# Performance work log

Hardware: AMD Instinct MI355X
Metric: run time of the kernel (lower is better)

## Reference

```python
import jax, jax.numpy as jnp
import numpy as np
import math

N, E = 1000, 128000
IN_DIM, HID, OUT_DIM = 256, 512, 16
L, H = 6, 8
C = HID // H  # 64, TransformerConv out_channels per head
EDGE_DIM = 32
MAX_LEN = 1000


def _pe(max_len, d_model):
    pos = np.arange(max_len)[:, None].astype(np.float32)
    div = np.exp(np.arange(0, d_model, 2).astype(np.float32) * (-math.log(10000.0) / d_model))
    pe = np.zeros((max_len, d_model), dtype=np.float32)
    pe[:, 0::2] = np.sin(pos * div)
    pe[:, 1::2] = np.cos(pos * div)
    return jnp.asarray(pe)


def setup_inputs() -> dict:
    key = jax.random.key(0)
    ks = jax.random.split(key, 32)
    g = lambda k, shape, fan_in: jax.random.normal(k, shape, jnp.float32) / jnp.sqrt(jnp.float32(fan_in))
    inp = {
        "x": jax.random.normal(ks[0], (N, IN_DIM), jnp.float32),
        "edge_index": jax.random.randint(ks[1], (2, E), 0, N, jnp.int64 if jax.config.jax_enable_x64 else jnp.int32),
        "edge_attr": jax.random.uniform(ks[2], (E, 4), jnp.float32),
        "embed_w": g(ks[3], (IN_DIM, HID), IN_DIM),
        "embed_b": jnp.zeros((HID,), jnp.float32),
        "pe": _pe(MAX_LEN, HID),
        "ee_w1": g(ks[4], (4, 16), 4), "ee_b1": jnp.zeros((16,), jnp.float32),
        "ee_w2": g(ks[5], (16, EDGE_DIM), 16), "ee_b2": jnp.zeros((EDGE_DIM,), jnp.float32),
        "q_w": g(ks[6], (L, HID, HID), HID), "q_b": jnp.zeros((L, HID), jnp.float32),
        "k_w": g(ks[7], (L, HID, HID), HID), "k_b": jnp.zeros((L, HID), jnp.float32),
        "v_w": g(ks[8], (L, HID, HID), HID), "v_b": jnp.zeros((L, HID), jnp.float32),
        "e_w": g(ks[9], (L, EDGE_DIM, HID), EDGE_DIM),
        "skip_w": g(ks[10], (L, HID, HID), HID), "skip_b": jnp.zeros((L, HID), jnp.float32),
        "ln_g": jnp.ones((L, HID), jnp.float32), "ln_b": jnp.zeros((L, HID), jnp.float32),
        "dom_w": g(ks[11], (HID, 16), HID), "dom_b": jnp.zeros((16,), jnp.float32),
        "cls_w1": g(ks[12], (HID + 16, HID // 2), HID + 16), "cls_b1": jnp.zeros((HID // 2,), jnp.float32),
        "cls_w2": g(ks[13], (HID // 2, OUT_DIM), HID // 2), "cls_b2": jnp.zeros((OUT_DIM,), jnp.float32),
    }
    return inp


def _layer_norm(x, g, b, eps=1e-5):
    mu = jnp.mean(x, axis=-1, keepdims=True)
    var = jnp.var(x, axis=-1, keepdims=True)
    return (x - mu) * jax.lax.rsqrt(var + eps) * g + b


def _forward(x, edge_index, edge_attr, embed_w, embed_b, pe, ee_w1, ee_b1, ee_w2, ee_b2,
             q_w, q_b, k_w, k_b, v_w, v_b, e_w, skip_w, skip_b, ln_g, ln_b,
             dom_w, dom_b, cls_w1, cls_b1, cls_w2, cls_b2):
    n = x.shape[0]
    h = x @ embed_w + embed_b
    h = h + pe[:n]
    # edge encoder: 4 -> 16 -> 32
    ef = jax.nn.relu(edge_attr @ ee_w1 + ee_b1) @ ee_w2 + ee_b2  # [E, 32]
    src, tgt = edge_index[0], edge_index[1]
    scale = 1.0 / math.sqrt(C)
    for l in range(L):
        res = h
        q = (h @ q_w[l] + q_b[l]).reshape(n, H, C)
        k = (h @ k_w[l] + k_b[l]).reshape(n, H, C)
        v = (h @ v_w[l] + v_b[l]).reshape(n, H, C)
        e = (ef @ e_w[l]).reshape(-1, H, C)            # [E, H, C], lin_edge has no bias
        kj = k[src] + e                                 # gather + edge bias
        score = jnp.sum(q[tgt] * kj, axis=-1) * scale   # [E, H]
        # segment softmax over incoming edges of each target node
        m = jax.ops.segment_max(score, tgt, num_segments=n)     # [N, H]
        al = jnp.exp(score - m[tgt])
        den = jax.ops.segment_sum(al, tgt, num_segments=n)      # [N, H]
        al = al / den[tgt]
        msg = (v[src] + e) * al[:, :, None]             # [E, H, C]
        out = jax.ops.segment_sum(msg, tgt, num_segments=n).reshape(n, HID)
        out = out + h @ skip_w[l] + skip_b[l]           # root_weight skip
        h = _layer_norm(out + res, ln_g[l], ln_b[l])
    dom = h @ dom_w + dom_b                             # [N, 16]
    comb = jnp.concatenate([h, dom], axis=-1)
    hid = jax.nn.relu(comb @ cls_w1 + cls_b1)
    return hid @ cls_w2 + cls_b2


def reference(x, edge_index, edge_attr, embed_w, embed_b, pe, ee_w1, ee_b1, ee_w2, ee_b2,
              q_w, q_b, k_w, k_b, v_w, v_b, e_w, skip_w, skip_b, ln_g, ln_b,
              dom_w, dom_b, cls_w1, cls_b1, cls_w2, cls_b2):
    return _forward(x, edge_index, edge_attr, embed_w, embed_b, pe, ee_w1, ee_b1, ee_w2, ee_b2,
                    q_w, q_b, k_w, k_b, v_w, v_b, e_w, skip_w, skip_b, ln_g, ln_b,
                    dom_w, dom_b, cls_w1, cls_b1, cls_w2, cls_b2)
```

## Files before the change

### kernel.cpp

```cpp
#include <hip/hip_runtime.h>
#include <hip/hip_bf16.h>
#include <cstdint>
#include <cstddef>

#define NN 1000
#define EE 128000
#define LAYERS 6
#define SCALE 0.125f
#define MAXDEG 320

typedef __attribute__((ext_vector_type(4))) float f32x4;
typedef __attribute__((ext_vector_type(8))) short short8v;

static __device__ __forceinline__ unsigned short f2bf(float x){
    unsigned int u = __float_as_uint(x);
    unsigned int lsb = (u >> 16) & 1u;
    u += 0x7fffu + lsb;
    return (unsigned short)(u >> 16);
}

__global__ void zero_counts(int* cnt){
    cnt[threadIdx.x] = 0;
}

__global__ void hist_kernel(const int* __restrict__ tgt, int* cnt){
    int e = blockIdx.x*256 + threadIdx.x;
    if (e < EE) atomicAdd(&cnt[tgt[e]], 1);
}

__global__ void scan_kernel(const int* __restrict__ cnt, int* offs, int* cursor){
    __shared__ int s[1024];
    int tid = threadIdx.x;
    s[tid] = (tid < NN) ? cnt[tid] : 0;
    __syncthreads();
    for (int st = 1; st < 1024; st <<= 1){
        int v = (tid >= st) ? s[tid-st] : 0;
        __syncthreads();
        s[tid] += v;
        __syncthreads();
    }
    int excl = (tid == 0) ? 0 : s[tid-1];
    if (tid < NN){ offs[tid] = excl; cursor[tid] = excl; }
    if (tid == 0) offs[NN] = s[NN-1];
}

__global__ void scatter_kernel(const int* __restrict__ src, const int* __restrict__ tgt,
                               int* cursor, int* ssrc, int* epos){
    int e = blockIdx.x*256 + threadIdx.x;
    if (e < EE){
        int t = tgt[e];
        int pos = atomicAdd(&cursor[t], 1);
        ssrc[pos] = src[e];
        epos[e] = pos;
    }
}

__global__ __launch_bounds__(256) void edge_enc(
    const float* __restrict__ edge_attr,
    const float* __restrict__ w1, const float* __restrict__ b1,
    const float* __restrict__ w2, const float* __restrict__ b2,
    const int* __restrict__ epos,
    float* __restrict__ efs)
{
    __shared__ float w1s[64], b1s[16], w2s[512], b2s[32];
    int tid = threadIdx.x;
    if (tid < 64) w1s[tid] = w1[tid];
    if (tid < 16) b1s[tid] = b1[tid];
    if (tid < 32) b2s[tid] = b2[tid];
    w2s[tid] = w2[tid];
    w2s[tid+256] = w2[tid+256];
    __syncthreads();
    int e = blockIdx.x*256 + tid;
    if (e >= EE) return;
    float4 av = *(const float4*)(edge_attr + (size_t)e*4);
    float hd[16];
    #pragma unroll
    for (int i = 0; i < 16; i++){
        float v = av.x*w1s[i] + av.y*w1s[16+i] + av.z*w1s[32+i] + av.w*w1s[48+i] + b1s[i];
        hd[i] = fmaxf(v, 0.f);
    }
    float outv[32];
    #pragma unroll
    for (int k = 0; k < 32; k++){
        float v = b2s[k];
        #pragma unroll
        for (int i = 0; i < 16; i++) v += hd[i]*w2s[i*32+k];
        outv[k] = v;
    }
    float* op = efs + (size_t)epos[e]*32;
    #pragma unroll
    for (int k4 = 0; k4 < 8; k4++){
        *(float4*)(op + k4*4) = make_float4(outv[k4*4], outv[k4*4+1], outv[k4*4+2], outv[k4*4+3]);
    }
}

__global__ __launch_bounds__(256) void convert_x(const float* __restrict__ x, unsigned short* __restrict__ xb){
    int row = blockIdx.x;
    int c = threadIdx.x;
    xb[(size_t)row*256 + c] = (row < NN) ? f2bf(x[(size_t)row*256 + c]) : (unsigned short)0;
}

__global__ __launch_bounds__(256) void tconv(const float* __restrict__ src, unsigned short* __restrict__ dst,
                                             int Kk, int Nn){
    int tn = blockIdx.x, tk = blockIdx.y;
    __shared__ float ts[32][33];
    int tid = threadIdx.x;
    int r = tid >> 3, c0 = (tid & 7)*4;
    float4 v = *(const float4*)(src + (size_t)(tk*32 + r)*Nn + tn*32 + c0);
    ts[r][c0+0] = v.x; ts[r][c0+1] = v.y; ts[r][c0+2] = v.z; ts[r][c0+3] = v.w;
    __syncthreads();
    ushort4 o;
    o.x = f2bf(ts[c0+0][r]); o.y = f2bf(ts[c0+1][r]);
    o.z = f2bf(ts[c0+2][r]); o.w = f2bf(ts[c0+3][r]);
    *(ushort4*)(dst + (size_t)(tn*32 + r)*Kk + tk*32 + c0) = o;
}

__global__ __launch_bounds__(256) void tconv24(
    const float* __restrict__ Wq, const float* __restrict__ Wk,
    const float* __restrict__ Wv, const float* __restrict__ Ws,
    unsigned short* __restrict__ Wt)
{
    int bid = blockIdx.x;
    int mm = bid >> 8;
    int tile = bid & 255;
    int tk = tile >> 4, tn = tile & 15;
    int l = mm >> 2, m = mm & 3;
    const float* W = ((m==0)?Wq:(m==1)?Wk:(m==2)?Wv:Ws) + (size_t)l*512*512;
    unsigned short* dst = Wt + (size_t)mm*512*512;
    __shared__ float ts[32][33];
    int tid = threadIdx.x;
    int r = tid >> 3, c0 = (tid & 7)*4;
    float4 v = *(const float4*)(W + (size_t)(tk*32 + r)*512 + tn*32 + c0);
    ts[r][c0+0] = v.x; ts[r][c0+1] = v.y; ts[r][c0+2] = v.z; ts[r][c0+3] = v.w;
    __syncthreads();
    ushort4 o;
    o.x = f2bf(ts[c0+0][r]); o.y = f2bf(ts[c0+1][r]);
    o.z = f2bf(ts[c0+2][r]); o.w = f2bf(ts[c0+3][r]);
    *(ushort4*)(dst + (size_t)(tn*32 + r)*512 + tk*32 + c0) = o;
}

__global__ __launch_bounds__(256) void gemm_embed_mfma(
    const unsigned short* __restrict__ xb,
    const unsigned short* __restrict__ ewt,
    const float* __restrict__ bias, const float* __restrict__ pe,
    float* __restrict__ C, unsigned short* __restrict__ hb)
{
    int bid = blockIdx.x;
    int mt = bid >> 2, nt = bid & 3;
    int row0 = mt*64, col0 = nt*128;

    __shared__ __align__(16) unsigned short As[64*40];
    __shared__ __align__(16) unsigned short Bs[128*40];

    int tid = threadIdx.x;
    int wid = tid >> 6, l = tid & 63;
    int wm = wid >> 1, wn = wid & 1;

    f32x4 acc[2][4] = {};
    int ar = tid >> 2, akq = tid & 3;
    for (int k0 = 0; k0 < 256; k0 += 32){
        *(uint4*)&As[ar*40 + akq*8]      = *(const uint4*)&xb[(size_t)(row0+ar)*256 + k0 + akq*8];
        *(uint4*)&Bs[ar*40 + akq*8]      = *(const uint4*)&ewt[(size_t)(col0+ar)*256 + k0 + akq*8];
        *(uint4*)&Bs[(ar+64)*40 + akq*8] = *(const uint4*)&ewt[(size_t)(col0+ar+64)*256 + k0 + akq*8];
        __syncthreads();
        short8v a0 = *(const short8v*)&As[(wm*32 + (l&15))*40 + (l>>4)*8];
        short8v a1 = *(const short8v*)&As[(wm*32 + 16 + (l&15))*40 + (l>>4)*8];
        #pragma unroll
        for (int nj = 0; nj < 4; nj++){
            short8v b = *(const short8v*)&Bs[(wn*64 + nj*16 + (l&15))*40 + (l>>4)*8];
            acc[0][nj] = __builtin_amdgcn_mfma_f32_16x16x32_bf16(a0, b, acc[0][nj], 0, 0, 0);
            acc[1][nj] = __builtin_amdgcn_mfma_f32_16x16x32_bf16(a1, b, acc[1][nj], 0, 0, 0);
        }
        __syncthreads();
    }
    int rbase = (l >> 4)*4, cl = l & 15;
    #pragma unroll
    for (int mi = 0; mi < 2; mi++)
        #pragma unroll
        for (int nj = 0; nj < 4; nj++)
            #pragma unroll
            for (int r = 0; r < 4; r++){
                int grow = row0 + wm*32 + mi*16 + rbase + r;
                int gcol = col0 + wn*64 + nj*16 + cl;
                if (grow < NN){
                    float v = acc[mi][nj][r] + bias[gcol] + pe[(size_t)grow*512 + gcol];
                    C[(size_t)grow*512 + gcol] = v;
                    hb[(size_t)grow*512 + gcol] = f2bf(v);
                }
            }
}

__global__ __launch_bounds__(256) void gemm_qkvs_mfma(
    const unsigned short* __restrict__ hb,
    const unsigned short* __restrict__ Wt,
    const float* __restrict__ qb, const float* __restrict__ kb,
    const float* __restrict__ vb, const float* __restrict__ sb,
    float* __restrict__ Q, float* __restrict__ K,
    float* __restrict__ V, float* __restrict__ S)
{
    int bid = blockIdx.x;
    int mat = bid >> 6;
    int rem = bid & 63;
    int mt = rem >> 2, nt = rem & 3;
    int row0 = mt*64, col0 = nt*128;
    const unsigned short* W = Wt + (size_t)mat*512*512;
    const float* bias = (mat==0)?qb:(mat==1)?kb:(mat==2)?vb:sb;
    float* C = (mat==0)?Q:(mat==1)?K:(mat==2)?V:S;

    __shared__ __align__(16) unsigned short As[64*72];
    __shared__ __align__(16) unsigned short Bs[128*72];

    int tid = threadIdx.x;
    int wid = tid >> 6, l = tid & 63;
    int wm = wid >> 1, wn = wid & 1;

    f32x4 acc[2][4] = {};
    int ar = tid >> 2, ac = tid & 3;
    int br = tid >> 1, bc = tid & 1;
    for (int k0 = 0; k0 < 512; k0 += 64){
        *(uint4*)&As[ar*72 + ac*16 + 0] = *(const uint4*)&hb[(size_t)(row0+ar)*512 + k0 + ac*16 + 0];
        *(uint4*)&As[ar*72 + ac*16 + 8] = *(const uint4*)&hb[(size_t)(row0+ar)*512 + k0 + ac*16 + 8];
        #pragma unroll
        for (int j = 0; j < 4; j++)
            *(uint4*)&Bs[br*72 + bc*32 + j*8] = *(const uint4*)&W[(size_t)(col0+br)*512 + k0 + bc*32 + j*8];
        __syncthreads();
        #pragma unroll
        for (int ks = 0; ks < 64; ks += 32){
            short8v a0 = *(const short8v*)&As[(wm*32 + (l&15))*72 + ks + (l>>4)*8];
            short8v a1 = *(const short8v*)&As[(wm*32 + 16 + (l&15))*72 + ks + (l>>4)*8];
            #pragma unroll
            for (int nj = 0; nj < 4; nj++){
                short8v b = *(const short8v*)&Bs[(wn*64 + nj*16 + (l&15))*72 + ks + (l>>4)*8];
                acc[0][nj] = __builtin_amdgcn_mfma_f32_16x16x32_bf16(a0, b, acc[0][nj], 0, 0, 0);
                acc[1][nj] = __builtin_amdgcn_mfma_f32_16x16x32_bf16(a1, b, acc[1][nj], 0, 0, 0);
            }
        }
        __syncthreads();
    }
    int rbase = (l >> 4)*4, cl = l & 15;
    #pragma unroll
    for (int mi = 0; mi < 2; mi++)
        #pragma unroll
        for (int nj = 0; nj < 4; nj++)
            #pragma unroll
            for (int r = 0; r < 4; r++){
                int grow = row0 + wm*32 + mi*16 + rbase + r;
                int gcol = col0 + wn*64 + nj*16 + cl;
                if (grow < NN) C[(size_t)grow*512 + gcol] = acc[mi][nj][r] + bias[gcol];
            }
}

__global__ __launch_bounds__(512) void attn_layer(
    const float* __restrict__ hcur,
    const float* __restrict__ Qm, const float* __restrict__ Km,
    const float* __restrict__ Vm, const float* __restrict__ SKm,
    const float* __restrict__ efs, const float* __restrict__ e_w_l,
    const float* __restrict__ ln_g_l, const float* __restrict__ ln_b_l,
    const int* __restrict__ ssrc, const int* __restrict__ offs,
    float* __restrict__ hnext, unsigned short* __restrict__ hbn)
{
    int tid = threadIdx.x;
    int t = blockIdx.x;

    __shared__ float q_s[8*68];
    __shared__ float qe_s[8*36];
    __shared__ float sc_s[MAXDEG*8];
    __shared__ __align__(8) unsigned short efb_s[MAXDEG*32];
    __shared__ int   src_s[MAXDEG];
    __shared__ float pv_s[2048];
    __shared__ float pe_s[512];
    __shared__ float s_s[256];
    __shared__ float red[64], red2[64];
    __shared__ float m_s[8], d_s[8];

    q_s[(tid>>6)*68 + (tid&63)] = Qm[(size_t)t*512 + tid];
    __syncthreads();
    if (tid < 256){
        int hh = tid>>5, dd = tid&31;
        const float* wrow = e_w_l + (size_t)dd*512 + hh*64;
        const float* qh = q_s + hh*68;
        float a = 0.f;
        #pragma unroll
        for (int c = 0; c < 64; c++) a += qh[c]*wrow[c];
        qe_s[hh*36 + dd] = a;
    }
    int start = offs[t], deg = offs[t+1] - start;
    __syncthreads();

    int cw = tid >> 5, l = tid & 31;
    int h = l >> 2, sub = l & 3;
    const float4* qp4  = (const float4*)(q_s + h*68 + sub*16);
    const float4* qep4 = (const float4*)(qe_s + h*36 + sub*8);
    float4 qa0 = qp4[0], qa1 = qp4[1], qa2 = qp4[2], qa3 = qp4[3];
    float4 qe0 = qep4[0], qe1 = qep4[1];
    float lmax = -1e30f;
    for (int i = cw; i < deg; i += 16){
        int s = ssrc[start + i];
        if (l == 0) src_s[i] = s;
        const float4* kr = (const float4*)(Km + (size_t)s*512 + l*16);
        const float4* er = (const float4*)(efs + (size_t)(start+i)*32);
        float4 k0 = kr[0], k1 = kr[1], k2 = kr[2], k3 = kr[3];
        float4 e0 = er[sub*2], e1 = er[sub*2+1];
        float p;
        p  = qa0.x*k0.x + qa0.y*k0.y + qa0.z*k0.z + qa0.w*k0.w;
        p += qa1.x*k1.x + qa1.y*k1.y + qa1.z*k1.z + qa1.w*k1.w;
        p += qa2.x*k2.x + qa2.y*k2.y + qa2.z*k2.z + qa2.w*k2.w;
        p += qa3.x*k3.x + qa3.y*k3.y + qa3.z*k3.z + qa3.w*k3.w;
        p += qe0.x*e0.x + qe0.y*e0.y + qe0.z*e0.z + qe0.w*e0.w;
        p += qe1.x*e1.x + qe1.y*e1.y + qe1.z*e1.z + qe1.w*e1.w;
        p += __shfl_xor(p, 1);
        p += __shfl_xor(p, 2);
        p *= SCALE;
        lmax = fmaxf(lmax, p);
        if (sub == 0) sc_s[i*8 + h] = p;
        if (l < 8){
            float4 ev = er[l];
            ushort4 ub;
            ub.x = f2bf(ev.x); ub.y = f2bf(ev.y); ub.z = f2bf(ev.z); ub.w = f2bf(ev.w);
            *(ushort4*)&efb_s[i*32 + l*4] = ub;
        }
    }
    lmax = fmaxf(lmax, __shfl_xor(lmax, 32));
    if (((tid & 63) < 32) && sub == 0) red[(tid>>6)*8 + h] = lmax;
    __syncthreads();
    if (tid < 8){
        float m = red[tid];
        #pragma unroll
        for (int w = 1; w < 8; w++) m = fmaxf(m, red[w*8 + tid]);
        m_s[tid] = m;
    }
    __syncthreads();

    {
        int he = tid & 7, ie = tid >> 3;
        float mh = m_s[he];
        float den = 0.f;
        for (int i = ie; i < deg; i += 64){
            float al = __expf(sc_s[i*8 + he] - mh);
            sc_s[i*8 + he] = al;
            den += al;
        }
        den += __shfl_xor(den, 8);
        den += __shfl_xor(den, 16);
        den += __shfl_xor(den, 32);
        if ((tid & 63) < 8) red2[(tid>>6)*8 + (tid & 7)] = den;
    }
    __syncthreads();
    if (tid < 8){
        float d = 0.f;
        #pragma unroll
        for (int w = 0; w < 8; w++) d += red2[w*8 + tid];
        d_s[tid] = d;
    }
    __syncthreads();

    {
        int c4 = tid & 127, g = tid >> 7;
        int h2 = c4 >> 4;
        float4 acc = make_float4(0.f, 0.f, 0.f, 0.f);
        const float4* Vm4 = (const float4*)Vm;
        #pragma unroll 4
        for (int i = g; i < deg; i += 4){
            int s = src_s[i];
            float al = sc_s[i*8 + h2];
            float4 v = Vm4[(size_t)s*128 + c4];
            acc.x += al*v.x; acc.y += al*v.y; acc.z += al*v.z; acc.w += al*v.w;
        }
        *(float4*)&pv_s[g*512 + c4*4] = acc;
    }
    {
        int c2 = tid & 255, g2 = tid >> 8;
        int h3 = c2 >> 5, dd3 = c2 & 31;
        float accE = 0.f;
        #pragma unroll 8
        for (int i = g2; i < deg; i += 2){
            float al = sc_s[i*8 + h3];
            float ev = __uint_as_float(((unsigned)efb_s[i*32 + dd3]) << 16);
            accE += al * ev;
        }
        pe_s[g2*256 + c2] = accE;
    }
    __syncthreads();
    if (tid < 256){
        float dv = d_s[tid>>5];
        float invd = (dv > 0.f) ? 1.f/dv : 0.f;
        s_s[tid] = (pe_s[tid] + pe_s[256+tid]) * invd;
    }
    __syncthreads();

    int c = tid;
    int hh2 = c >> 6;
    float dv = d_s[hh2];
    float invd = (dv > 0.f) ? 1.f/dv : 0.f;
    float vtot = pv_s[c] + pv_s[512+c] + pv_s[1024+c] + pv_s[1536+c];
    float r = vtot * invd;
    float oe = 0.f;
    const float* sp = s_s + hh2*32;
    #pragma unroll
    for (int d = 0; d < 32; d++) oe += sp[d]*e_w_l[(size_t)d*512 + c];
    float x = r + oe + SKm[(size_t)t*512 + c] + hcur[(size_t)t*512 + c];

    int wv = tid >> 6, ln = tid & 63;
    float sA = x, sB = x*x;
    #pragma unroll
    for (int m2 = 1; m2 <= 32; m2 <<= 1){
        sA += __shfl_xor(sA, m2);
        sB += __shfl_xor(sB, m2);
    }
    if (ln == 0){ red[wv] = sA; red2[wv] = sB; }
    __syncthreads();
    float tot = 0.f, tot2 = 0.f;
    #pragma unroll
    for (int w = 0; w < 8; w++){ tot += red[w]; tot2 += red2[w]; }
    float mu  = tot*(1.f/512.f);
    float var = tot2*(1.f/512.f) - mu*mu;
    float rstd = rsqrtf(var + 1e-5f);
    float y = (x - mu)*rstd*ln_g_l[c] + ln_b_l[c];
    hnext[(size_t)t*512 + c] = y;
    hbn[(size_t)t*512 + c]   = f2bf(y);
}

__global__ __launch_bounds__(256) void final_head(
    const float* __restrict__ hin,
    const float* __restrict__ dom_w, const float* __restrict__ dom_b,
    const float* __restrict__ w1, const float* __restrict__ b1,
    const float* __restrict__ w2, const float* __restrict__ b2,
    float* __restrict__ out)
{
    int tid = threadIdx.x, t = blockIdx.x;
    __shared__ float h_s[512];
    __shared__ float dom_s[16];
    __shared__ float hid_s[256];
    __shared__ float red[256];
    h_s[tid]     = hin[(size_t)t*512 + tid];
    h_s[tid+256] = hin[(size_t)t*512 + 256 + tid];
    __syncthreads();
    if (tid < 16){
        float a = dom_b[tid];
        for (int i = 0; i < 512; i++) a += h_s[i]*dom_w[i*16 + tid];
        dom_s[tid] = a;
    }
    __syncthreads();
    float acc = b1[tid];
    for (int i = 0; i < 512; i++) acc += h_s[i]*w1[(size_t)i*256 + tid];
    #pragma unroll
    for (int i = 0; i < 16; i++) acc += dom_s[i]*w1[(size_t)(512+i)*256 + tid];
    hid_s[tid] = fmaxf(acc, 0.f);
    __syncthreads();
    int o = tid & 15, g = tid >> 4;
    float p = 0.f;
    #pragma unroll
    for (int j = 0; j < 16; j++) p += hid_s[g*16 + j]*w2[(g*16 + j)*16 + o];
    red[tid] = p;
    __syncthreads();
    if (tid < 16){
        float s2 = b2[tid];
        for (int gg = 0; gg < 16; gg++) s2 += red[gg*16 + tid];
        out[(size_t)t*16 + tid] = s2;
    }
}

extern "C" void kernel_launch(void* const* d_in, const int* in_sizes, int n_in,
                              void* d_out, int out_size, void* d_ws, size_t ws_size,
                              hipStream_t stream)
{
    const float* x       = (const float*)d_in[0];
    const int*   eidx    = (const int*)  d_in[1];
    const float* eattr   = (const float*)d_in[2];
    const float* embed_w = (const float*)d_in[3];
    const float* embed_b = (const float*)d_in[4];
    const float* pe      = (const float*)d_in[5];
    const float* ee_w1   = (const float*)d_in[6];
    const float* ee_b1   = (const float*)d_in[7];
    const float* ee_w2   = (const float*)d_in[8];
    const float* ee_b2   = (const float*)d_in[9];
    const float* q_w     = (const float*)d_in[10];
    const float* q_b     = (const float*)d_in[11];
    const float* k_w     = (const float*)d_in[12];
    const float* k_b     = (const float*)d_in[13];
    const float* v_w     = (const float*)d_in[14];
    const float* v_b     = (const float*)d_in[15];
    const float* e_w     = (const float*)d_in[16];
    const float* skip_w  = (const float*)d_in[17];
    const float* skip_b  = (const float*)d_in[18];
    const float* ln_g    = (const float*)d_in[19];
    const float* ln_b    = (const float*)d_in[20];
    const float* dom_w   = (const float*)d_in[21];
    const float* dom_b   = (const float*)d_in[22];
    const float* cls_w1  = (const float*)d_in[23];
    const float* cls_b1  = (const float*)d_in[24];
    const float* cls_w2  = (const float*)d_in[25];
    const float* cls_b2  = (const float*)d_in[26];
    float* out = (float*)d_out;

    float* ws = (float*)d_ws;
    size_t o = 0;
    float* h0    = ws + o; o += (size_t)512*NN;
    float* h1    = ws + o; o += (size_t)512*NN;
    float* Qb    = ws + o; o += (size_t)512*NN;
    float* Kb    = ws + o; o += (size_t)512*NN;
    float* Vb    = ws + o; o += (size_t)512*NN;
    float* Sb    = ws + o; o += (size_t)512*NN;
    float* efs   = ws + o; o += (size_t)32*EE;
    unsigned short* hb  = (unsigned short*)(ws + o); o += (size_t)1024*512/2;
    unsigned short* xb  = (unsigned short*)(ws + o); o += (size_t)1024*256/2;
    unsigned short* ewt = (unsigned short*)(ws + o); o += (size_t)512*256/2;
    unsigned short* Wtb = (unsigned short*)(ws + o); o += (size_t)24*512*512/2;
    int* cnt    = (int*)(ws + o); o += 1024;
    int* offs   = (int*)(ws + o); o += 1024;
    int* cursor = (int*)(ws + o); o += 1024;
    int* ssrc   = (int*)(ws + o); o += EE;
    int* epos   = (int*)(ws + o); o += EE;

    const int* srcp = eidx;
    const int* tgtp = eidx + EE;

    zero_counts<<<1, 1024, 0, stream>>>(cnt);
    hist_kernel<<<EE/256, 256, 0, stream>>>(tgtp, cnt);
    scan_kernel<<<1, 1024, 0, stream>>>(cnt, offs, cursor);
    scatter_kernel<<<EE/256, 256, 0, stream>>>(srcp, tgtp, cursor, ssrc, epos);
    edge_enc<<<EE/256, 256, 0, stream>>>(eattr, ee_w1, ee_b1, ee_w2, ee_b2, epos, efs);
    convert_x<<<1024, 256, 0, stream>>>(x, xb);
    tconv<<<dim3(512/32, 256/32), 256, 0, stream>>>(embed_w, ewt, 256, 512);
    tconv24<<<24*256, 256, 0, stream>>>(q_w, k_w, v_w, skip_w, Wtb);
    gemm_embed_mfma<<<64, 256, 0, stream>>>(xb, ewt, embed_b, pe, h0, hb);

    float* hc = h0;
    float* hn = h1;
    for (int l = 0; l < LAYERS; l++){
        gemm_qkvs_mfma<<<256, 256, 0, stream>>>(
            hb, Wtb + (size_t)l*4*512*512,
            q_b + (size_t)l*512, k_b + (size_t)l*512,
            v_b + (size_t)l*512, skip_b + (size_t)l*512,
            Qb, Kb, Vb, Sb);
        attn_layer<<<NN, 512, 0, stream>>>(
            hc, Qb, Kb, Vb, Sb, efs, e_w + (size_t)l*32*512,
            ln_g + (size_t)l*512, ln_b + (size_t)l*512,
            ssrc, offs, hn, hb);
        float* tmp = hc; hc = hn; hn = tmp;
    }
    final_head<<<NN, 256, 0, stream>>>(hc, dom_w, dom_b, cls_w1, cls_b1, cls_w2, cls_b2, out);
}
```

Measured before the change: 684.2 us.

## Store K, V and edge features in bf16; retile QKVS GEMM with register prefetch

K and V projections and the encoded edge features are now written as bf16 instead of fp32, halving the gather traffic in the attention kernel. The attention kernel also drops its shared-memory bf16 copy of edge features and reads them from global memory. The QKVS GEMM switches to 64x64 tiles with twice as many blocks and prefetches the next K-slice into registers. The cost is lower precision in K and V, which were previously fp32.

```diff
diff --git a/kernel.cpp b/kernel.cpp
--- a/kernel.cpp
+++ b/kernel.cpp
@@ -17,6 +17,9 @@
     unsigned int lsb = (u >> 16) & 1u;
     u += 0x7fffu + lsb;
     return (unsigned short)(u >> 16);
+}
+static __device__ __forceinline__ float bf2f(unsigned short u){
+    return __uint_as_float(((unsigned int)u) << 16);
 }
 
 __global__ void zero_counts(int* cnt){
@@ -60,7 +63,7 @@
     const float* __restrict__ w1, const float* __restrict__ b1,
     const float* __restrict__ w2, const float* __restrict__ b2,
     const int* __restrict__ epos,
-    float* __restrict__ efs)
+    unsigned short* __restrict__ efs)
 {
     __shared__ float w1s[64], b1s[16], w2s[512], b2s[32];
     int tid = threadIdx.x;
@@ -79,18 +82,21 @@
         float v = av.x*w1s[i] + av.y*w1s[16+i] + av.z*w1s[32+i] + av.w*w1s[48+i] + b1s[i];
         hd[i] = fmaxf(v, 0.f);
     }
-    float outv[32];
-    #pragma unroll
-    for (int k = 0; k < 32; k++){
-        float v = b2s[k];
-        #pragma unroll
-        for (int i = 0; i < 16; i++) v += hd[i]*w2s[i*32+k];
-        outv[k] = v;
-    }
-    float* op = efs + (size_t)epos[e]*32;
+    unsigned short* op = efs + (size_t)epos[e]*32;
     #pragma unroll
     for (int k4 = 0; k4 < 8; k4++){
-        *(float4*)(op + k4*4) = make_float4(outv[k4*4], outv[k4*4+1], outv[k4*4+2], outv[k4*4+3]);
+        ushort4 ub;
+        float v0 = b2s[k4*4+0], v1 = b2s[k4*4+1], v2 = b2s[k4*4+2], v3 = b2s[k4*4+3];
+        #pragma unroll
+        for (int i = 0; i < 16; i++){
+            float hv = hd[i];
+            v0 += hv*w2s[i*32 + k4*4+0];
+            v1 += hv*w2s[i*32 + k4*4+1];
+            v2 += hv*w2s[i*32 + k4*4+2];
+            v3 += hv*w2s[i*32 + k4*4+3];
+        }
+        ub.x = f2bf(v0); ub.y = f2bf(v1); ub.z = f2bf(v2); ub.w = f2bf(v3);
+        *(ushort4*)(op + k4*4) = ub;
     }
 }
 
@@ -195,66 +201,84 @@
     const unsigned short* __restrict__ Wt,
     const float* __restrict__ qb, const float* __restrict__ kb,
     const float* __restrict__ vb, const float* __restrict__ sb,
-    float* __restrict__ Q, float* __restrict__ K,
-    float* __restrict__ V, float* __restrict__ S)
+    float* __restrict__ Q, unsigned short* __restrict__ K16,
+    unsigned short* __restrict__ V16, float* __restrict__ S)
 {
     int bid = blockIdx.x;
-    int mat = bid >> 6;
-    int rem = bid & 63;
-    int mt = rem >> 2, nt = rem & 3;
-    int row0 = mt*64, col0 = nt*128;
+    int mat = bid >> 7;
+    int rem = bid & 127;
+    int mt = rem >> 3, nt = rem & 7;
+    int row0 = mt*64, col0 = nt*64;
     const unsigned short* W = Wt + (size_t)mat*512*512;
     const float* bias = (mat==0)?qb:(mat==1)?kb:(mat==2)?vb:sb;
-    float* C = (mat==0)?Q:(mat==1)?K:(mat==2)?V:S;
 
     __shared__ __align__(16) unsigned short As[64*72];
-    __shared__ __align__(16) unsigned short Bs[128*72];
+    __shared__ __align__(16) unsigned short Bs[64*72];
 
     int tid = threadIdx.x;
     int wid = tid >> 6, l = tid & 63;
     int wm = wid >> 1, wn = wid & 1;
 
-    f32x4 acc[2][4] = {};
-    int ar = tid >> 2, ac = tid & 3;
-    int br = tid >> 1, bc = tid & 1;
+    f32x4 acc[2][2] = {};
+    int lr = tid >> 2;
+    int lc = (tid & 3)*2;
+    const unsigned short* ga = hb + (size_t)(row0+lr)*512 + lc*8;
+    const unsigned short* gb = W  + (size_t)(col0+lr)*512 + lc*8;
+
+    uint4 ra0 = *(const uint4*)(ga);
+    uint4 ra1 = *(const uint4*)(ga + 8);
+    uint4 rb0 = *(const uint4*)(gb);
+    uint4 rb1 = *(const uint4*)(gb + 8);
+
     for (int k0 = 0; k0 < 512; k0 += 64){
-        *(uint4*)&As[ar*72 + ac*16 + 0] = *(const uint4*)&hb[(size_t)(row0+ar)*512 + k0 + ac*16 + 0];
-        *(uint4*)&As[ar*72 + ac*16 + 8] = *(const uint4*)&hb[(size_t)(row0+ar)*512 + k0 + ac*16 + 8];
-        #pragma unroll
-        for (int j = 0; j < 4; j++)
-            *(uint4*)&Bs[br*72 + bc*32 + j*8] = *(const uint4*)&W[(size_t)(col0+br)*512 + k0 + bc*32 + j*8];
         __syncthreads();
-        #pragma unroll
-        for (int ks = 0; ks < 64; ks += 32){
-            short8v a0 = *(const short8v*)&As[(wm*32 + (l&15))*72 + ks + (l>>4)*8];
-            short8v a1 = *(const short8v*)&As[(wm*32 + 16 + (l&15))*72 + ks + (l>>4)*8];
-            #pragma unroll
-            for (int nj = 0; nj < 4; nj++){
-                short8v b = *(const short8v*)&Bs[(wn*64 + nj*16 + (l&15))*72 + ks + (l>>4)*8];
-                acc[0][nj] = __builtin_amdgcn_mfma_f32_16x16x32_bf16(a0, b, acc[0][nj], 0, 0, 0);
-                acc[1][nj] = __builtin_amdgcn_mfma_f32_16x16x32_bf16(a1, b, acc[1][nj], 0, 0, 0);
-            }
-        }
+        *(uint4*)&As[lr*72 + lc*8]     = ra0;
+        *(uint4*)&As[lr*72 + lc*8 + 8] = ra1;
+        *(uint4*)&Bs[lr*72 + lc*8]     = rb0;
+        *(uint4*)&Bs[lr*72 + lc*8 + 8] = rb1;
         __syncthreads();
+        if (k0 + 64 < 512){
+            ra0 = *(const uint4*)(ga + k0 + 64);
+            ra1 = *(const uint4*)(ga + k0 + 72);
+            rb0 = *(const uint4*)(gb + k0 + 64);
+            rb1 = *(const uint4*)(gb + k0 + 72);
+        }
+        #pragma unroll
+        for (int ks = 0; ks < 2; ks++){
+            short8v a0 = *(const short8v*)&As[(wm*32 + (l&15))*72      + ks*32 + (l>>4)*8];
+            short8v a1 = *(const short8v*)&As[(wm*32 + 16 + (l&15))*72 + ks*32 + (l>>4)*8];
+            short8v b0 = *(const short8v*)&Bs[(wn*32 + (l&15))*72      + ks*32 + (l>>4)*8];
+            short8v b1 = *(const short8v*)&Bs[(wn*32 + 16 + (l&15))*72 + ks*32 + (l>>4)*8];
+            acc[0][0] = __builtin_amdgcn_mfma_f32_16x16x32_bf16(a0, b0, acc[0][0], 0, 0, 0);
+            acc[0][1] = __builtin_amdgcn_mfma_f32_16x16x32_bf16(a0, b1, acc[0][1], 0, 0, 0);
+            acc[1][0] = __builtin_amdgcn_mfma_f32_16x16x32_bf16(a1, b0, acc[1][0], 0, 0, 0);
+            acc[1][1] = __builtin_amdgcn_mfma_f32_16x16x32_bf16(a1, b1, acc[1][1], 0, 0, 0);
+        }
     }
     int rbase = (l >> 4)*4, cl = l & 15;
     #pragma unroll
     for (int mi = 0; mi < 2; mi++)
         #pragma unroll
-        for (int nj = 0; nj < 4; nj++)
+        for (int nj = 0; nj < 2; nj++)
             #pragma unroll
             for (int r = 0; r < 4; r++){
                 int grow = row0 + wm*32 + mi*16 + rbase + r;
-                int gcol = col0 + wn*64 + nj*16 + cl;
-                if (grow < NN) C[(size_t)grow*512 + gcol] = acc[mi][nj][r] + bias[gcol];
+                int gcol = col0 + wn*32 + nj*16 + cl;
+                if (grow < NN){
+                    float v = acc[mi][nj][r] + bias[gcol];
+                    if (mat == 0)      Q[(size_t)grow*512 + gcol] = v;
+                    else if (mat == 1) K16[(size_t)grow*512 + gcol] = f2bf(v);
+                    else if (mat == 2) V16[(size_t)grow*512 + gcol] = f2bf(v);
+                    else               S[(size_t)grow*512 + gcol] = v;
+                }
             }
 }
 
 __global__ __launch_bounds__(512) void attn_layer(
     const float* __restrict__ hcur,
-    const float* __restrict__ Qm, const float* __restrict__ Km,
-    const float* __restrict__ Vm, const float* __restrict__ SKm,
-    const float* __restrict__ efs, const float* __restrict__ e_w_l,
+    const float* __restrict__ Qm, const unsigned short* __restrict__ Km,
+    const unsigned short* __restrict__ Vm, const float* __restrict__ SKm,
+    const unsigned short* __restrict__ efs, const float* __restrict__ e_w_l,
     const float* __restrict__ ln_g_l, const float* __restrict__ ln_b_l,
     const int* __restrict__ ssrc, const int* __restrict__ offs,
     float* __restrict__ hnext, unsigned short* __restrict__ hbn)
@@ -265,7 +289,6 @@
     __shared__ float q_s[8*68];
     __shared__ float qe_s[8*36];
     __shared__ float sc_s[MAXDEG*8];
-    __shared__ __align__(8) unsigned short efb_s[MAXDEG*32];
     __shared__ int   src_s[MAXDEG];
     __shared__ float pv_s[2048];
     __shared__ float pe_s[512];
@@ -297,28 +320,28 @@
     for (int i = cw; i < deg; i += 16){
         int s = ssrc[start + i];
         if (l == 0) src_s[i] = s;
-        const float4* kr = (const float4*)(Km + (size_t)s*512 + l*16);
-        const float4* er = (const float4*)(efs + (size_t)(start+i)*32);
-        float4 k0 = kr[0], k1 = kr[1], k2 = kr[2], k3 = kr[3];
-        float4 e0 = er[sub*2], e1 = er[sub*2+1];
+        const unsigned short* kr = Km + (size_t)s*512 + l*16;
+        short8v k0 = *(const short8v*)(kr);
+        short8v k1 = *(const short8v*)(kr + 8);
+        short8v ev = *(const short8v*)(efs + (size_t)(start+i)*32 + sub*8);
         float p;
-        p  = qa0.x*k0.x + qa0.y*k0.y + qa0.z*k0.z + qa0.w*k0.w;
-        p += qa1.x*k1.x + qa1.y*k1.y + qa1.z*k1.z + qa1.w*k1.w;
-        p += qa2.x*k2.x + qa2.y*k2.y + qa2.z*k2.z + qa2.w*k2.w;
-        p += qa3.x*k3.x + qa3.y*k3.y + qa3.z*k3.z + qa3.w*k3.w;
-        p += qe0.x*e0.x + qe0.y*e0.y + qe0.z*e0.z + qe0.w*e0.w;
-        p += qe1.x*e1.x + qe1.y*e1.y + qe1.z*e1.z + qe1.w*e1.w;
+        p  = qa0.x*bf2f((unsigned short)k0[0]) + qa0.y*bf2f((unsigned short)k0[1])
+           + qa0.z*bf2f((unsigned short)k0[2]) + qa0.w*bf2f((unsigned short)k0[3]);
+        p += qa1.x*bf2f((unsigned short)k0[4]) + qa1.y*bf2f((unsigned short)k0[5])
+           + qa1.z*bf2f((unsigned short)k0[6]) + qa1.w*bf2f((unsigned short)k0[7]);
+        p += qa2.x*bf2f((unsigned short)k1[0]) + qa2.y*bf2f((unsigned short)k1[1])
+           + qa2.z*bf2f((unsigned short)k1[2]) + qa2.w*bf2f((unsigned short)k1[3]);
+        p += qa3.x*bf2f((unsigned short)k1[4]) + qa3.y*bf2f((unsigned short)k1[5])
+           + qa3.z*bf2f((unsigned short)k1[6]) + qa3.w*bf2f((unsigned short)k1[7]);
+        p += qe0.x*bf2f((unsigned short)ev[0]) + qe0.y*bf2f((unsigned short)ev[1])
+           + qe0.z*bf2f((unsigned short)ev[2]) + qe0.w*bf2f((unsigned short)ev[3]);
+        p += qe1.x*bf2f((unsigned short)ev[4]) + qe1.y*bf2f((unsigned short)ev[5])
+           + qe1.z*bf2f((unsigned short)ev[6]) + qe1.w*bf2f((unsigned short)ev[7]);
         p += __shfl_xor(p, 1);
         p += __shfl_xor(p, 2);
         p *= SCALE;
         lmax = fmaxf(lmax, p);
         if (sub == 0) sc_s[i*8 + h] = p;
-        if (l < 8){
-            float4 ev = er[l];
-            ushort4 ub;
-            ub.x = f2bf(ev.x); ub.y = f2bf(ev.y); ub.z = f2bf(ev.z); ub.w = f2bf(ev.w);
-            *(ushort4*)&efb_s[i*32 + l*4] = ub;
-        }
     }
     lmax = fmaxf(lmax, __shfl_xor(lmax, 32));
     if (((tid & 63) < 32) && sub == 0) red[(tid>>6)*8 + h] = lmax;
@@ -358,13 +381,13 @@
         int c4 = tid & 127, g = tid >> 7;
         int h2 = c4 >> 4;
         float4 acc = make_float4(0.f, 0.f, 0.f, 0.f);
-        const float4* Vm4 = (const float4*)Vm;
         #pragma unroll 4
         for (int i = g; i < deg; i += 4){
             int s = src_s[i];
             float al = sc_s[i*8 + h2];
-            float4 v = Vm4[(size_t)s*128 + c4];
-            acc.x += al*v.x; acc.y += al*v.y; acc.z += al*v.z; acc.w += al*v.w;
+            ushort4 v = *(const ushort4*)(Vm + (size_t)s*512 + c4*4);
+            acc.x += al*bf2f(v.x); acc.y += al*bf2f(v.y);
+            acc.z += al*bf2f(v.z); acc.w += al*bf2f(v.w);
         }
         *(float4*)&pv_s[g*512 + c4*4] = acc;
     }
@@ -375,8 +398,7 @@
         #pragma unroll 8
         for (int i = g2; i < deg; i += 2){
             float al = sc_s[i*8 + h3];
-            float ev = __uint_as_float(((unsigned)efb_s[i*32 + dd3]) << 16);
-            accE += al * ev;
+            accE += al * bf2f(efs[(size_t)(start+i)*32 + dd3]);
         }
         pe_s[g2*256 + c2] = accE;
     }
@@ -498,14 +520,14 @@
     float* h0    = ws + o; o += (size_t)512*NN;
     float* h1    = ws + o; o += (size_t)512*NN;
     float* Qb    = ws + o; o += (size_t)512*NN;
-    float* Kb    = ws + o; o += (size_t)512*NN;
-    float* Vb    = ws + o; o += (size_t)512*NN;
     float* Sb    = ws + o; o += (size_t)512*NN;
-    float* efs   = ws + o; o += (size_t)32*EE;
-    unsigned short* hb  = (unsigned short*)(ws + o); o += (size_t)1024*512/2;
-    unsigned short* xb  = (unsigned short*)(ws + o); o += (size_t)1024*256/2;
-    unsigned short* ewt = (unsigned short*)(ws + o); o += (size_t)512*256/2;
-    unsigned short* Wtb = (unsigned short*)(ws + o); o += (size_t)24*512*512/2;
+    unsigned short* Kb16 = (unsigned short*)(ws + o); o += (size_t)1024*512/2;
+    unsigned short* Vb16 = (unsigned short*)(ws + o); o += (size_t)1024*512/2;
+    unsigned short* efs  = (unsigned short*)(ws + o); o += (size_t)EE*32/2;
+    unsigned short* hb   = (unsigned short*)(ws + o); o += (size_t)1024*512/2;
+    unsigned short* xb   = (unsigned short*)(ws + o); o += (size_t)1024*256/2;
+    unsigned short* ewt  = (unsigned short*)(ws + o); o += (size_t)512*256/2;
+    unsigned short* Wtb  = (unsigned short*)(ws + o); o += (size_t)24*512*512/2;
     int* cnt    = (int*)(ws + o); o += 1024;
     int* offs   = (int*)(ws + o); o += 1024;
     int* cursor = (int*)(ws + o); o += 1024;
@@ -528,13 +550,13 @@
     float* hc = h0;
     float* hn = h1;
     for (int l = 0; l < LAYERS; l++){
-        gemm_qkvs_mfma<<<256, 256, 0, stream>>>(
+        gemm_qkvs_mfma<<<512, 256, 0, stream>>>(
             hb, Wtb + (size_t)l*4*512*512,
             q_b + (size_t)l*512, k_b + (size_t)l*512,
             v_b + (size_t)l*512, skip_b + (size_t)l*512,
-            Qb, Kb, Vb, Sb);
+            Qb, Kb16, Vb16, Sb);
         attn_layer<<<NN, 512, 0, stream>>>(
-            hc, Qb, Kb, Vb, Sb, efs, e_w + (size_t)l*32*512,
+            hc, Qb, Kb16, Vb16, Sb, efs, e_w + (size_t)l*32*512,
             ln_g + (size_t)l*512, ln_b + (size_t)l*512,
             ssrc, offs, hn, hb);
         float* tmp = hc; hc = hn; hn = tmp;
```

New measurement: 581.1 us. 1.18x faster.
